# Performance work log

Hardware: AMD Instinct MI355X
Metric: run time of the kernel (lower is better)

Reference implementation:

```python
import jax, jax.numpy as jnp
import numpy as np

B, N, NODE_DIM, EDGE_DIM, HID = 32, 100, 128, 64, 128
EPS = 1e-5


def _bn(x, gamma, beta):
    # training-mode BatchNorm1d over all leading dims (biased variance)
    d = x.shape[-1]
    xf = x.reshape(-1, d)
    mean = xf.mean(axis=0)
    var = ((xf - mean) ** 2).mean(axis=0)
    return ((x - mean) * jax.lax.rsqrt(var + EPS)) * gamma + beta


def setup_inputs() -> dict:
    key = jax.random.key(0)
    ks = jax.random.split(key, 12)
    s = lambda fan_in: 1.0 / np.sqrt(fan_in)
    return {
        "h": jax.random.normal(ks[0], (B, N, NODE_DIM), jnp.float32),
        "e": jax.random.normal(ks[1], (B, N, N, EDGE_DIM), jnp.float32),
        "adj": (jax.random.uniform(ks[2], (B, N, N)) < 0.3).astype(jnp.float32),
        "WU": jax.random.uniform(ks[3], (HID, NODE_DIM), jnp.float32, -s(NODE_DIM), s(NODE_DIM)),
        "WV": jax.random.uniform(ks[4], (HID, NODE_DIM), jnp.float32, -s(NODE_DIM), s(NODE_DIM)),
        "WA": jax.random.uniform(ks[5], (HID, NODE_DIM), jnp.float32, -s(NODE_DIM), s(NODE_DIM)),
        "WB": jax.random.uniform(ks[6], (HID, NODE_DIM), jnp.float32, -s(NODE_DIM), s(NODE_DIM)),
        "WC": jax.random.uniform(ks[7], (HID, EDGE_DIM), jnp.float32, -s(EDGE_DIM), s(EDGE_DIM)),
        "bn_edge_gamma": jnp.ones((HID,), jnp.float32),
        "bn_edge_beta": jnp.zeros((HID,), jnp.float32),
        "bn_node_gamma": jnp.ones((HID,), jnp.float32),
        "bn_node_beta": jnp.zeros((HID,), jnp.float32),
    }


def reference(h, e, adj, WU, WV, WA, WB, WC,
              bn_edge_gamma, bn_edge_beta, bn_node_gamma, bn_node_beta):
    # e_new[b,m,n,d] = C(e) + A(h_m) + B(h_n)
    eh = (jnp.einsum('bmne,de->bmnd', e, WC)
          + jnp.einsum('bmc,dc->bmd', h, WA)[:, :, None, :]
          + jnp.einsum('bnc,dc->bnd', h, WB)[:, None, :, :])
    eh = jax.nn.relu(_bn(eh, bn_edge_gamma, bn_edge_beta))
    eh = eh * adj[..., None]
    e_weight = jax.nn.sigmoid(eh)
    e_norm = jax.nn.softmax(e_weight, axis=2)  # softmax over neighbor dim n
    h_in = jnp.einsum('bmc,dc->bmd', h, WU)
    h_nb = jnp.einsum('bnc,dc->bnd', h, WV)
    m = jnp.einsum('bmnd,bnd->bmd', e_norm, h_nb)
    m = _bn(m, bn_node_gamma, bn_node_beta)
    h_out = h_in + jax.nn.relu(m)
    return (h_out, e_norm)
```

## Files before the change

kernel.cpp:

```cpp
#include <hip/hip_runtime.h>
#include <math.h>

#define B_   32
#define N_   100
#define ND_  128
#define ED_  64
#define HID_ 128
#define EPS_ 1e-5f
#define NNODE (B_*N_)
#define EDGE_SAMPLES ((float)(B_*N_*N_))
#define LOG2E_ 1.4426950408889634f

#define MC_     7

#define WS_A      0
#define WS_PK     409600
#define WS_HIN    819200
#define WS_M      1638400
#define WS_STATS  2048000
#define WS_SCSH   (WS_STATS + 8192)
#define WS_NSTB   (WS_SCSH + 256)
#define ZERO_CNT  (8192 + 256 + 8192)

typedef __attribute__((ext_vector_type(8))) short bf16x8;
typedef __attribute__((ext_vector_type(4))) float f32x4;
#define MFMA16(a,b,c) __builtin_amdgcn_mfma_f32_16x16x32_bf16(a,b,c,0,0,0)

__device__ __forceinline__ unsigned short f2bf(float f) {
  unsigned int u = __float_as_uint(f);
  unsigned int r = (u + 0x7fffu + ((u >> 16) & 1u)) >> 16;
  return (unsigned short)r;
}

__global__ __launch_bounds__(256) void k1_proj(
    const float* __restrict__ h,
    const float* __restrict__ WA, const float* __restrict__ WB,
    const float* __restrict__ WU, const float* __restrict__ WV,
    float* __restrict__ ws) {
  __shared__ unsigned short h_lds[128 * 136];
  __shared__ unsigned short w_lds[128 * 136];
  const int t  = threadIdx.x;
  const int r0 = blockIdx.x * 128;
  const int y  = blockIdx.y;
  const float* W = (y == 0) ? WA : (y == 1) ? WB : (y == 2) ? WU : WV;

  {
    int gid = (y * 25 + blockIdx.x) * 256 + t;
    if (gid < ZERO_CNT) ws[WS_STATS + gid] = 0.f;
  }

  const float4* hp = (const float4*)(h + (size_t)r0 * 128);
  const float4* wp = (const float4*)W;
#pragma unroll
  for (int k = 0; k < 16; ++k) {
    int i = t + k * 256;
    int row = i >> 5, col = (i & 31) * 4;
    float4 v = hp[i];
    *(ushort4*)&h_lds[row * 136 + col] =
        make_ushort4(f2bf(v.x), f2bf(v.y), f2bf(v.z), f2bf(v.w));
    float4 u = wp[i];
    *(ushort4*)&w_lds[row * 136 + col] =
        make_ushort4(f2bf(u.x), f2bf(u.y), f2bf(u.z), f2bf(u.w));
  }
  __syncthreads();

  const int w  = t >> 6;
  const int l  = t & 63;
  const int lr = l & 15;
  const int lg = l >> 4;

  bf16x8 bfr[2][4];
#pragma unroll
  for (int nt = 0; nt < 2; ++nt) {
    int d = w * 32 + nt * 16 + lr;
#pragma unroll
    for (int kb = 0; kb < 4; ++kb)
      bfr[nt][kb] = *(const bf16x8*)&w_lds[d * 136 + kb * 32 + lg * 8];
  }

  f32x4 acc[8][2];
#pragma unroll
  for (int mt = 0; mt < 8; ++mt) { acc[mt][0] = (f32x4)0.f; acc[mt][1] = (f32x4)0.f; }

#pragma unroll
  for (int mt = 0; mt < 8; ++mt) {
    int row = mt * 16 + lr;
    bf16x8 af[4];
#pragma unroll
    for (int kb = 0; kb < 4; ++kb)
      af[kb] = *(const bf16x8*)&h_lds[row * 136 + kb * 32 + lg * 8];
#pragma unroll
    for (int nt = 0; nt < 2; ++nt)
#pragma unroll
      for (int kb = 0; kb < 4; ++kb)
        acc[mt][nt] = MFMA16(af[kb], bfr[nt][kb], acc[mt][nt]);
  }

  if (y == 0 || y == 2) {
    float* outp = ws + ((y == 0) ? WS_A : WS_HIN);
#pragma unroll
    for (int mt = 0; mt < 8; ++mt)
#pragma unroll
      for (int nt = 0; nt < 2; ++nt) {
        int dcol = w * 32 + nt * 16 + lr;
#pragma unroll
        for (int j = 0; j < 4; ++j) {
          int row = r0 + mt * 16 + lg * 4 + j;
          outp[row * 128 + dcol] = acc[mt][nt][j];
        }
      }
  } else {
    unsigned short* pks = (unsigned short*)(ws + WS_PK);
    const int half = (y == 1) ? 0 : 1;
#pragma unroll
    for (int mt = 0; mt < 8; ++mt)
#pragma unroll
      for (int nt = 0; nt < 2; ++nt) {
        int dcol = w * 32 + nt * 16 + lr;
#pragma unroll
        for (int j = 0; j < 4; ++j) {
          int row = r0 + mt * 16 + lg * 4 + j;
          pks[(row * 128 + dcol) * 2 + half] = f2bf(acc[mt][nt][j]);
        }
      }
  }
}

__global__ __launch_bounds__(256, 1) void k2_stats(
    const float* __restrict__ e, const float* __restrict__ WC,
    float* __restrict__ ws) {
  __shared__ unsigned short wc_lds[128 * 72];
  __shared__ unsigned short e_lds[2][112 * 72];
  const int t     = threadIdx.x;
  const int b     = blockIdx.x;
  const int chunk = blockIdx.y;
  const int m0    = chunk * MC_;
  const int mcnt  = min(MC_, N_ - m0);

  const float4* wcp = (const float4*)WC;
#pragma unroll
  for (int k = 0; k < 8; ++k) {
    int i = t + k * 256;
    float4 v = wcp[i];
    int row = i >> 4, col = (i & 15) * 4;
    *(ushort4*)&wc_lds[row * 72 + col] =
        make_ushort4(f2bf(v.x), f2bf(v.y), f2bf(v.z), f2bf(v.w));
  }
  for (int i = t; i < 12 * 72; i += 256) {
    e_lds[0][100 * 72 + i] = 0;
    e_lds[1][100 * 72 + i] = 0;
  }

  const int w  = t >> 6;
  const int l  = t & 63;
  const int lr = l & 15;
  const int lg = l >> 4;
  const int d0 = w * 32 + lr, d1 = d0 + 16;

  unsigned int pk0[7][4], pk1[7][4];
  const unsigned int* pkp = (const unsigned int*)(ws + WS_PK) + b * (N_ * 128);
#pragma unroll
  for (int mt = 0; mt < 7; ++mt)
#pragma unroll
    for (int j = 0; j < 4; ++j) {
      int node = mt * 16 + lg * 4 + j;
      bool ok = node < N_;
      pk0[mt][j] = ok ? pkp[node * 128 + d0] : 0u;
      pk1[mt][j] = ok ? pkp[node * 128 + d1] : 0u;
    }
  __syncthreads();

  bf16x8 bfr[2][2];
#pragma unroll
  for (int nt = 0; nt < 2; ++nt) {
    int d = w * 32 + nt * 16 + lr;
#pragma unroll
    for (int kb = 0; kb < 2; ++kb)
      bfr[nt][kb] = *(const bf16x8*)&wc_lds[d * 72 + kb * 32 + lg * 8];
  }

  float4 ld[7];
  {
    const float4* epf4 = (const float4*)(e + (size_t)(b * N_ + m0) * (N_ * ED_));
#pragma unroll
    for (int k = 0; k < 7; ++k) { int i = t + k * 256; if (i < 1600) ld[k] = epf4[i]; }
  }

  float s0 = 0.f, ss0 = 0.f, s1 = 0.f, ss1 = 0.f;
  int buf = 0;
  for (int r = 0; r < mcnt; ++r) {
#pragma unroll
    for (int k = 0; k < 7; ++k) {
      int i = t + k * 256;
      if (i < 1600) {
        float4 v = ld[k];
        int row = i >> 4, col = (i & 15) * 4;
        *(ushort4*)&e_lds[buf][row * 72 + col] =
            make_ushort4(f2bf(v.x), f2bf(v.y), f2bf(v.z), f2bf(v.w));
      }
    }
    __syncthreads();
    if (r + 1 < mcnt) {
      const float4* nxt = (const float4*)(e + (size_t)(b * N_ + m0 + r + 1) * (N_ * ED_));
#pragma unroll
      for (int k = 0; k < 7; ++k) { int i = t + k * 256; if (i < 1600) ld[k] = nxt[i]; }
    }

    const int bm = b * N_ + m0 + r;
    const float A0 = ws[WS_A + bm * 128 + d0];
    const float A1 = ws[WS_A + bm * 128 + d1];

    f32x4 acc[7][2];
#pragma unroll
    for (int mt = 0; mt < 7; ++mt) { acc[mt][0] = (f32x4)0.f; acc[mt][1] = (f32x4)0.f; }
#pragma unroll
    for (int mt = 0; mt < 7; ++mt) {
      int row = mt * 16 + lr;
      bf16x8 af0 = *(const bf16x8*)&e_lds[buf][row * 72 + lg * 8];
      bf16x8 af1 = *(const bf16x8*)&e_lds[buf][row * 72 + 32 + lg * 8];
#pragma unroll
      for (int nt = 0; nt < 2; ++nt) {
        acc[mt][nt] = MFMA16(af0, bfr[nt][0], acc[mt][nt]);
        acc[mt][nt] = MFMA16(af1, bfr[nt][1], acc[mt][nt]);
      }
    }

#pragma unroll
    for (int mt = 0; mt < 7; ++mt)
#pragma unroll
      for (int j = 0; j < 4; ++j) {
        int node = mt * 16 + lg * 4 + j;
        if (node < N_) {
          float x0 = acc[mt][0][j] + A0 + __uint_as_float(pk0[mt][j] << 16);
          float x1 = acc[mt][1][j] + A1 + __uint_as_float(pk1[mt][j] << 16);
          s0 += x0; ss0 += x0 * x0;
          s1 += x1; ss1 += x1 * x1;
        }
      }
    buf ^= 1;
  }

  s0 += __shfl_xor(s0, 16);  s0 += __shfl_xor(s0, 32);
  ss0 += __shfl_xor(ss0, 16); ss0 += __shfl_xor(ss0, 32);
  s1 += __shfl_xor(s1, 16);  s1 += __shfl_xor(s1, 32);
  ss1 += __shfl_xor(ss1, 16); ss1 += __shfl_xor(ss1, 32);
  if (l < 16) {
    atomicAdd(&ws[WS_STATS + b * 256 + d0], s0);
    atomicAdd(&ws[WS_STATS + b * 256 + 128 + d0], ss0);
    atomicAdd(&ws[WS_STATS + b * 256 + d1], s1);
    atomicAdd(&ws[WS_STATS + b * 256 + 128 + d1], ss1);
  }
}

__global__ __launch_bounds__(128) void k0_finalize(
    const float* __restrict__ gamma_e, const float* __restrict__ beta_e,
    float* __restrict__ ws) {
  const int t = threadIdx.x;
  float S = 0.f, SS = 0.f;
#pragma unroll
  for (int j = 0; j < 32; ++j) {
    S  += ws[WS_STATS + j * 256 + t];
    SS += ws[WS_STATS + j * 256 + 128 + t];
  }
  float mean = S * (1.0f / EDGE_SAMPLES);
  float var  = SS * (1.0f / EDGE_SAMPLES) - mean * mean;
  float sc   = gamma_e[t] * rsqrtf(var + EPS_);
  ws[WS_SCSH + t]       = sc;
  ws[WS_SCSH + 128 + t] = beta_e[t] - mean * sc;
}

__global__ __launch_bounds__(512) void k4_main(
    const float* __restrict__ e, const float* __restrict__ adj,
    const float* __restrict__ WC,
    float* __restrict__ ws, float* __restrict__ out_enorm) {
  __shared__ unsigned short e_lds[112 * 72];
  __shared__ float adj_lds[112];
  const int t  = threadIdx.x;
  const int bm = blockIdx.x;
  const int b  = bm / N_;
  const int w  = t >> 6;
  const int l  = t & 63;
  const int lr = l & 15;
  const int lg = l >> 4;
  const int d0 = w * 16 + lr;

  float4 ld[4];
  const float4* ef4 = (const float4*)(e + (size_t)bm * (N_ * ED_));
#pragma unroll
  for (int k = 0; k < 4; ++k) { int i = t + k * 512; if (i < 1600) ld[k] = ef4[i]; }

  unsigned int pk[7][4];
  const unsigned int* pkp = (const unsigned int*)(ws + WS_PK) + b * (N_ * 128);
#pragma unroll
  for (int mt = 0; mt < 7; ++mt)
#pragma unroll
    for (int j = 0; j < 4; ++j) {
      int node = mt * 16 + lg * 4 + j;
      pk[mt][j] = (node < N_) ? pkp[node * 128 + d0] : 0u;
    }
  const float A0  = ws[WS_A + bm * 128 + d0];
  const float sc0 = ws[WS_SCSH + d0];
  const float sh0 = ws[WS_SCSH + 128 + d0];

  bf16x8 bfr[2];
#pragma unroll
  for (int kb = 0; kb < 2; ++kb) {
    const float* wrow = WC + d0 * 64 + kb * 32 + lg * 8;
    float4 u0 = *(const float4*)wrow;
    float4 u1 = *(const float4*)(wrow + 4);
    bf16x8 f;
    f[0] = (short)f2bf(u0.x); f[1] = (short)f2bf(u0.y);
    f[2] = (short)f2bf(u0.z); f[3] = (short)f2bf(u0.w);
    f[4] = (short)f2bf(u1.x); f[5] = (short)f2bf(u1.y);
    f[6] = (short)f2bf(u1.z); f[7] = (short)f2bf(u1.w);
    bfr[kb] = f;
  }

  if (t < 112) adj_lds[t] = (t < N_) ? adj[bm * N_ + t] : 0.f;

#pragma unroll
  for (int k = 0; k < 4; ++k) {
    int i = t + k * 512;
    if (i < 1600) {
      float4 v = ld[k];
      int row = i >> 4, col = (i & 15) * 4;
      *(ushort4*)&e_lds[row * 72 + col] =
          make_ushort4(f2bf(v.x), f2bf(v.y), f2bf(v.z), f2bf(v.w));
    }
  }
  for (int i = t; i < 12 * 72; i += 512) e_lds[100 * 72 + i] = 0;
  __syncthreads();

  f32x4 acc[7];
#pragma unroll
  for (int mt = 0; mt < 7; ++mt) acc[mt] = (f32x4)0.f;
#pragma unroll
  for (int mt = 0; mt < 7; ++mt) {
    int row = mt * 16 + lr;
    bf16x8 af0 = *(const bf16x8*)&e_lds[row * 72 + lg * 8];
    bf16x8 af1 = *(const bf16x8*)&e_lds[row * 72 + 32 + lg * 8];
    acc[mt] = MFMA16(af0, bfr[0], acc[mt]);
    acc[mt] = MFMA16(af1, bfr[1], acc[mt]);
  }

  float den = 0.f;
#pragma unroll
  for (int mt = 0; mt < 7; ++mt)
#pragma unroll
    for (int j = 0; j < 4; ++j) {
      int node = mt * 16 + lg * 4 + j;
      float bv = __uint_as_float(pk[mt][j] << 16);
      float x  = (acc[mt][j] + A0 + bv) * sc0 + sh0;
      float r  = fmaxf(x, 0.f) * adj_lds[node];
      float en = __builtin_amdgcn_exp2f(r * -LOG2E_);
      float sg = __builtin_amdgcn_rcpf(1.f + en);
      float p  = __builtin_amdgcn_exp2f(sg * LOG2E_);
      acc[mt][j] = p; den += p;
    }
  den += __shfl_xor(den, 16); den += __shfl_xor(den, 32);
  den -= 12.f * __builtin_amdgcn_exp2f(0.5f * LOG2E_);
  const float rc = __builtin_amdgcn_rcpf(den);

  float msg = 0.f;
  float* outp = out_enorm + (size_t)bm * (N_ * 128);
#pragma unroll
  for (int mt = 0; mt < 7; ++mt)
#pragma unroll
    for (int j = 0; j < 4; ++j) {
      int node = mt * 16 + lg * 4 + j;
      if (node < N_) {
        float v = acc[mt][j] * rc;
        outp[node * 128 + d0] = v;
        float hn = __uint_as_float(pk[mt][j] & 0xffff0000u);
        msg += v * hn;
      }
    }
  msg += __shfl_xor(msg, 16); msg += __shfl_xor(msg, 32);
  if (l < 16) {
    ws[WS_M + bm * 128 + d0] = msg;
    atomicAdd(&ws[WS_NSTB + b * 256 + d0],       msg);
    atomicAdd(&ws[WS_NSTB + b * 256 + 128 + d0], msg * msg);
  }
}

__global__ __launch_bounds__(256) void k5b_hout(
    const float* __restrict__ gamma_n, const float* __restrict__ beta_n,
    const float* __restrict__ ws, float* __restrict__ hout) {
  __shared__ float sc_l[128], sh_l[128];
  const int t = threadIdx.x;
  if (t < 128) {
    float S = 0.f, SS = 0.f;
#pragma unroll
    for (int j = 0; j < 32; ++j) {
      S  += ws[WS_NSTB + j * 256 + t];
      SS += ws[WS_NSTB + j * 256 + 128 + t];
    }
    float mean = S * (1.0f / (float)NNODE);
    float var  = SS * (1.0f / (float)NNODE) - mean * mean;
    float sc   = gamma_n[t] * rsqrtf(var + EPS_);
    sc_l[t] = sc;
    sh_l[t] = beta_n[t] - mean * sc;
  }
  __syncthreads();
  const int idx = blockIdx.x * 256 + t;
  const int d = t & 127;
  float mv = ws[WS_M + idx];
  hout[idx] = ws[WS_HIN + idx] + fmaxf(mv * sc_l[d] + sh_l[d], 0.f);
}

extern "C" void kernel_launch(void* const* d_in, const int* in_sizes, int n_in,
                              void* d_out, int out_size, void* d_ws, size_t ws_size,
                              hipStream_t stream) {
  (void)in_sizes; (void)n_in; (void)out_size; (void)ws_size;
  const float* h   = (const float*)d_in[0];
  const float* e   = (const float*)d_in[1];
  const float* adj = (const float*)d_in[2];
  const float* WU  = (const float*)d_in[3];
  const float* WV  = (const float*)d_in[4];
  const float* WA  = (const float*)d_in[5];
  const float* WB  = (const float*)d_in[6];
  const float* WC  = (const float*)d_in[7];
  const float* geg = (const float*)d_in[8];
  const float* geb = (const float*)d_in[9];
  const float* gng = (const float*)d_in[10];
  const float* gnb = (const float*)d_in[11];

  float* out = (float*)d_out;
  float* ws  = (float*)d_ws;

  k1_proj    <<<dim3(25, 4),  256, 0, stream>>>(h, WA, WB, WU, WV, ws);
  k2_stats   <<<dim3(32, 15), 256, 0, stream>>>(e, WC, ws);
  k0_finalize<<<1,            128, 0, stream>>>(geg, geb, ws);
  k4_main    <<<3200,         512, 0, stream>>>(e, adj, WC, ws, out + 409600);
  k5b_hout   <<<1600,         256, 0, stream>>>(gng, gnb, ws, out);
}
```

Measured before the change: 89.09 us.

## Regrid stats and projection kernels for more parallelism and swizzle main block order

The stats kernel changes from 480 blocks of 256 threads, each looping over 7 rows with both 32-wide halves of the hidden dimension per wave, to 1600 blocks of 512 threads that each handle two rows with 16 hidden columns per wave. WC is loaded straight from global memory rather than staged through LDS. The projection kernel halves its row tile to 64 so it launches twice as many blocks. The main kernel remaps block indices in a strided swizzle across batches, meant to spread work across XCDs and caches. The aim is better occupancy and latency hiding on the bandwidth-bound pass over e, at the cost of more blocks, more redundant loads of pk, A and WC, and more atomics.

```diff
diff --git a/kernel.cpp b/kernel.cpp
--- a/kernel.cpp
+++ b/kernel.cpp
@@ -11,8 +11,6 @@
 #define EDGE_SAMPLES ((float)(B_*N_*N_))
 #define LOG2E_ 1.4426950408889634f
 
-#define MC_     7
-
 #define WS_A      0
 #define WS_PK     409600
 #define WS_HIN    819200
@@ -32,277 +30,8 @@
   return (unsigned short)r;
 }
 
-__global__ __launch_bounds__(256) void k1_proj(
-    const float* __restrict__ h,
-    const float* __restrict__ WA, const float* __restrict__ WB,
-    const float* __restrict__ WU, const float* __restrict__ WV,
-    float* __restrict__ ws) {
-  __shared__ unsigned short h_lds[128 * 136];
-  __shared__ unsigned short w_lds[128 * 136];
-  const int t  = threadIdx.x;
-  const int r0 = blockIdx.x * 128;
-  const int y  = blockIdx.y;
-  const float* W = (y == 0) ? WA : (y == 1) ? WB : (y == 2) ? WU : WV;
-
-  {
-    int gid = (y * 25 + blockIdx.x) * 256 + t;
-    if (gid < ZERO_CNT) ws[WS_STATS + gid] = 0.f;
-  }
-
-  const float4* hp = (const float4*)(h + (size_t)r0 * 128);
-  const float4* wp = (const float4*)W;
-#pragma unroll
-  for (int k = 0; k < 16; ++k) {
-    int i = t + k * 256;
-    int row = i >> 5, col = (i & 31) * 4;
-    float4 v = hp[i];
-    *(ushort4*)&h_lds[row * 136 + col] =
-        make_ushort4(f2bf(v.x), f2bf(v.y), f2bf(v.z), f2bf(v.w));
-    float4 u = wp[i];
-    *(ushort4*)&w_lds[row * 136 + col] =
-        make_ushort4(f2bf(u.x), f2bf(u.y), f2bf(u.z), f2bf(u.w));
-  }
-  __syncthreads();
-
-  const int w  = t >> 6;
-  const int l  = t & 63;
-  const int lr = l & 15;
-  const int lg = l >> 4;
-
-  bf16x8 bfr[2][4];
-#pragma unroll
-  for (int nt = 0; nt < 2; ++nt) {
-    int d = w * 32 + nt * 16 + lr;
-#pragma unroll
-    for (int kb = 0; kb < 4; ++kb)
-      bfr[nt][kb] = *(const bf16x8*)&w_lds[d * 136 + kb * 32 + lg * 8];
-  }
-
-  f32x4 acc[8][2];
-#pragma unroll
-  for (int mt = 0; mt < 8; ++mt) { acc[mt][0] = (f32x4)0.f; acc[mt][1] = (f32x4)0.f; }
-
-#pragma unroll
-  for (int mt = 0; mt < 8; ++mt) {
-    int row = mt * 16 + lr;
-    bf16x8 af[4];
-#pragma unroll
-    for (int kb = 0; kb < 4; ++kb)
-      af[kb] = *(const bf16x8*)&h_lds[row * 136 + kb * 32 + lg * 8];
-#pragma unroll
-    for (int nt = 0; nt < 2; ++nt)
-#pragma unroll
-      for (int kb = 0; kb < 4; ++kb)
-        acc[mt][nt] = MFMA16(af[kb], bfr[nt][kb], acc[mt][nt]);
-  }
-
-  if (y == 0 || y == 2) {
-    float* outp = ws + ((y == 0) ? WS_A : WS_HIN);
-#pragma unroll
-    for (int mt = 0; mt < 8; ++mt)
-#pragma unroll
-      for (int nt = 0; nt < 2; ++nt) {
-        int dcol = w * 32 + nt * 16 + lr;
-#pragma unroll
-        for (int j = 0; j < 4; ++j) {
-          int row = r0 + mt * 16 + lg * 4 + j;
-          outp[row * 128 + dcol] = acc[mt][nt][j];
-        }
-      }
-  } else {
-    unsigned short* pks = (unsigned short*)(ws + WS_PK);
-    const int half = (y == 1) ? 0 : 1;
-#pragma unroll
-    for (int mt = 0; mt < 8; ++mt)
-#pragma unroll
-      for (int nt = 0; nt < 2; ++nt) {
-        int dcol = w * 32 + nt * 16 + lr;
-#pragma unroll
-        for (int j = 0; j < 4; ++j) {
-          int row = r0 + mt * 16 + lg * 4 + j;
-          pks[(row * 128 + dcol) * 2 + half] = f2bf(acc[mt][nt][j]);
-        }
-      }
-  }
-}
-
-__global__ __launch_bounds__(256, 1) void k2_stats(
-    const float* __restrict__ e, const float* __restrict__ WC,
-    float* __restrict__ ws) {
-  __shared__ unsigned short wc_lds[128 * 72];
-  __shared__ unsigned short e_lds[2][112 * 72];
-  const int t     = threadIdx.x;
-  const int b     = blockIdx.x;
-  const int chunk = blockIdx.y;
-  const int m0    = chunk * MC_;
-  const int mcnt  = min(MC_, N_ - m0);
-
-  const float4* wcp = (const float4*)WC;
-#pragma unroll
-  for (int k = 0; k < 8; ++k) {
-    int i = t + k * 256;
-    float4 v = wcp[i];
-    int row = i >> 4, col = (i & 15) * 4;
-    *(ushort4*)&wc_lds[row * 72 + col] =
-        make_ushort4(f2bf(v.x), f2bf(v.y), f2bf(v.z), f2bf(v.w));
-  }
-  for (int i = t; i < 12 * 72; i += 256) {
-    e_lds[0][100 * 72 + i] = 0;
-    e_lds[1][100 * 72 + i] = 0;
-  }
-
-  const int w  = t >> 6;
-  const int l  = t & 63;
-  const int lr = l & 15;
-  const int lg = l >> 4;
-  const int d0 = w * 32 + lr, d1 = d0 + 16;
-
-  unsigned int pk0[7][4], pk1[7][4];
-  const unsigned int* pkp = (const unsigned int*)(ws + WS_PK) + b * (N_ * 128);
-#pragma unroll
-  for (int mt = 0; mt < 7; ++mt)
-#pragma unroll
-    for (int j = 0; j < 4; ++j) {
-      int node = mt * 16 + lg * 4 + j;
-      bool ok = node < N_;
-      pk0[mt][j] = ok ? pkp[node * 128 + d0] : 0u;
-      pk1[mt][j] = ok ? pkp[node * 128 + d1] : 0u;
-    }
-  __syncthreads();
-
-  bf16x8 bfr[2][2];
-#pragma unroll
-  for (int nt = 0; nt < 2; ++nt) {
-    int d = w * 32 + nt * 16 + lr;
-#pragma unroll
-    for (int kb = 0; kb < 2; ++kb)
-      bfr[nt][kb] = *(const bf16x8*)&wc_lds[d * 72 + kb * 32 + lg * 8];
-  }
-
-  float4 ld[7];
-  {
-    const float4* epf4 = (const float4*)(e + (size_t)(b * N_ + m0) * (N_ * ED_));
-#pragma unroll
-    for (int k = 0; k < 7; ++k) { int i = t + k * 256; if (i < 1600) ld[k] = epf4[i]; }
-  }
-
-  float s0 = 0.f, ss0 = 0.f, s1 = 0.f, ss1 = 0.f;
-  int buf = 0;
-  for (int r = 0; r < mcnt; ++r) {
-#pragma unroll
-    for (int k = 0; k < 7; ++k) {
-      int i = t + k * 256;
-      if (i < 1600) {
-        float4 v = ld[k];
-        int row = i >> 4, col = (i & 15) * 4;
-        *(ushort4*)&e_lds[buf][row * 72 + col] =
-            make_ushort4(f2bf(v.x), f2bf(v.y), f2bf(v.z), f2bf(v.w));
-      }
-    }
-    __syncthreads();
-    if (r + 1 < mcnt) {
-      const float4* nxt = (const float4*)(e + (size_t)(b * N_ + m0 + r + 1) * (N_ * ED_));
-#pragma unroll
-      for (int k = 0; k < 7; ++k) { int i = t + k * 256; if (i < 1600) ld[k] = nxt[i]; }
-    }
-
-    const int bm = b * N_ + m0 + r;
-    const float A0 = ws[WS_A + bm * 128 + d0];
-    const float A1 = ws[WS_A + bm * 128 + d1];
-
-    f32x4 acc[7][2];
-#pragma unroll
-    for (int mt = 0; mt < 7; ++mt) { acc[mt][0] = (f32x4)0.f; acc[mt][1] = (f32x4)0.f; }
-#pragma unroll
-    for (int mt = 0; mt < 7; ++mt) {
-      int row = mt * 16 + lr;
-      bf16x8 af0 = *(const bf16x8*)&e_lds[buf][row * 72 + lg * 8];
-      bf16x8 af1 = *(const bf16x8*)&e_lds[buf][row * 72 + 32 + lg * 8];
-#pragma unroll
-      for (int nt = 0; nt < 2; ++nt) {
-        acc[mt][nt] = MFMA16(af0, bfr[nt][0], acc[mt][nt]);
-        acc[mt][nt] = MFMA16(af1, bfr[nt][1], acc[mt][nt]);
-      }
-    }
-
-#pragma unroll
-    for (int mt = 0; mt < 7; ++mt)
-#pragma unroll
-      for (int j = 0; j < 4; ++j) {
-        int node = mt * 16 + lg * 4 + j;
-        if (node < N_) {
-          float x0 = acc[mt][0][j] + A0 + __uint_as_float(pk0[mt][j] << 16);
-          float x1 = acc[mt][1][j] + A1 + __uint_as_float(pk1[mt][j] << 16);
-          s0 += x0; ss0 += x0 * x0;
-          s1 += x1; ss1 += x1 * x1;
-        }
-      }
-    buf ^= 1;
-  }
-
-  s0 += __shfl_xor(s0, 16);  s0 += __shfl_xor(s0, 32);
-  ss0 += __shfl_xor(ss0, 16); ss0 += __shfl_xor(ss0, 32);
-  s1 += __shfl_xor(s1, 16);  s1 += __shfl_xor(s1, 32);
-  ss1 += __shfl_xor(ss1, 16); ss1 += __shfl_xor(ss1, 32);
-  if (l < 16) {
-    atomicAdd(&ws[WS_STATS + b * 256 + d0], s0);
-    atomicAdd(&ws[WS_STATS + b * 256 + 128 + d0], ss0);
-    atomicAdd(&ws[WS_STATS + b * 256 + d1], s1);
-    atomicAdd(&ws[WS_STATS + b * 256 + 128 + d1], ss1);
-  }
-}
-
-__global__ __launch_bounds__(128) void k0_finalize(
-    const float* __restrict__ gamma_e, const float* __restrict__ beta_e,
-    float* __restrict__ ws) {
-  const int t = threadIdx.x;
-  float S = 0.f, SS = 0.f;
-#pragma unroll
-  for (int j = 0; j < 32; ++j) {
-    S  += ws[WS_STATS + j * 256 + t];
-    SS += ws[WS_STATS + j * 256 + 128 + t];
-  }
-  float mean = S * (1.0f / EDGE_SAMPLES);
-  float var  = SS * (1.0f / EDGE_SAMPLES) - mean * mean;
-  float sc   = gamma_e[t] * rsqrtf(var + EPS_);
-  ws[WS_SCSH + t]       = sc;
-  ws[WS_SCSH + 128 + t] = beta_e[t] - mean * sc;
-}
-
-__global__ __launch_bounds__(512) void k4_main(
-    const float* __restrict__ e, const float* __restrict__ adj,
-    const float* __restrict__ WC,
-    float* __restrict__ ws, float* __restrict__ out_enorm) {
-  __shared__ unsigned short e_lds[112 * 72];
-  __shared__ float adj_lds[112];
-  const int t  = threadIdx.x;
-  const int bm = blockIdx.x;
-  const int b  = bm / N_;
-  const int w  = t >> 6;
-  const int l  = t & 63;
-  const int lr = l & 15;
-  const int lg = l >> 4;
-  const int d0 = w * 16 + lr;
-
-  float4 ld[4];
-  const float4* ef4 = (const float4*)(e + (size_t)bm * (N_ * ED_));
-#pragma unroll
-  for (int k = 0; k < 4; ++k) { int i = t + k * 512; if (i < 1600) ld[k] = ef4[i]; }
-
-  unsigned int pk[7][4];
-  const unsigned int* pkp = (const unsigned int*)(ws + WS_PK) + b * (N_ * 128);
-#pragma unroll
-  for (int mt = 0; mt < 7; ++mt)
-#pragma unroll
-    for (int j = 0; j < 4; ++j) {
-      int node = mt * 16 + lg * 4 + j;
-      pk[mt][j] = (node < N_) ? pkp[node * 128 + d0] : 0u;
-    }
-  const float A0  = ws[WS_A + bm * 128 + d0];
-  const float sc0 = ws[WS_SCSH + d0];
-  const float sh0 = ws[WS_SCSH + 128 + d0];
-
-  bf16x8 bfr[2];
+__device__ __forceinline__ void load_wc_frags(const float* __restrict__ WC,
+                                              int d0, int lg, bf16x8 bfr[2]) {
 #pragma unroll
   for (int kb = 0; kb < 2; ++kb) {
     const float* wrow = WC + d0 * 64 + kb * 32 + lg * 8;
@@ -315,33 +44,278 @@
     f[6] = (short)f2bf(u1.z); f[7] = (short)f2bf(u1.w);
     bfr[kb] = f;
   }
-
-  if (t < 112) adj_lds[t] = (t < N_) ? adj[bm * N_ + t] : 0.f;
-
+}
+
+__device__ __forceinline__ void stage_row512(const float4 ld[4],
+                                             unsigned short* dst, int t) {
 #pragma unroll
   for (int k = 0; k < 4; ++k) {
     int i = t + k * 512;
     if (i < 1600) {
       float4 v = ld[k];
       int row = i >> 4, col = (i & 15) * 4;
-      *(ushort4*)&e_lds[row * 72 + col] =
+      *(ushort4*)&dst[row * 72 + col] =
           make_ushort4(f2bf(v.x), f2bf(v.y), f2bf(v.z), f2bf(v.w));
     }
   }
+}
+
+__device__ __forceinline__ void mfma_row(const unsigned short* src,
+                                         const bf16x8 bfr[2], f32x4 acc[7],
+                                         int lr, int lg) {
+#pragma unroll
+  for (int mt = 0; mt < 7; ++mt) {
+    int row = mt * 16 + lr;
+    bf16x8 af0 = *(const bf16x8*)&src[row * 72 + lg * 8];
+    bf16x8 af1 = *(const bf16x8*)&src[row * 72 + 32 + lg * 8];
+    f32x4 a = (f32x4)0.f;
+    a = MFMA16(af0, bfr[0], a);
+    a = MFMA16(af1, bfr[1], a);
+    acc[mt] = a;
+  }
+}
+
+__global__ __launch_bounds__(256) void k1_proj(
+    const float* __restrict__ h,
+    const float* __restrict__ WA, const float* __restrict__ WB,
+    const float* __restrict__ WU, const float* __restrict__ WV,
+    float* __restrict__ ws) {
+  __shared__ unsigned short h_lds[64 * 136];
+  __shared__ unsigned short w_lds[128 * 136];
+  const int t  = threadIdx.x;
+  const int r0 = blockIdx.x * 64;
+  const int y  = blockIdx.y;
+  const float* W = (y == 0) ? WA : (y == 1) ? WB : (y == 2) ? WU : WV;
+
+  {
+    int gid = (y * 50 + blockIdx.x) * 256 + t;
+    if (gid < ZERO_CNT) ws[WS_STATS + gid] = 0.f;
+  }
+
+  const float4* hp = (const float4*)(h + (size_t)r0 * 128);
+  const float4* wp = (const float4*)W;
+#pragma unroll
+  for (int k = 0; k < 8; ++k) {
+    int i = t + k * 256;
+    int row = i >> 5, col = (i & 31) * 4;
+    float4 v = hp[i];
+    *(ushort4*)&h_lds[row * 136 + col] =
+        make_ushort4(f2bf(v.x), f2bf(v.y), f2bf(v.z), f2bf(v.w));
+  }
+#pragma unroll
+  for (int k = 0; k < 16; ++k) {
+    int i = t + k * 256;
+    int row = i >> 5, col = (i & 31) * 4;
+    float4 u = wp[i];
+    *(ushort4*)&w_lds[row * 136 + col] =
+        make_ushort4(f2bf(u.x), f2bf(u.y), f2bf(u.z), f2bf(u.w));
+  }
+  __syncthreads();
+
+  const int w  = t >> 6;
+  const int l  = t & 63;
+  const int lr = l & 15;
+  const int lg = l >> 4;
+
+  bf16x8 bfr[2][4];
+#pragma unroll
+  for (int nt = 0; nt < 2; ++nt) {
+    int d = w * 32 + nt * 16 + lr;
+#pragma unroll
+    for (int kb = 0; kb < 4; ++kb)
+      bfr[nt][kb] = *(const bf16x8*)&w_lds[d * 136 + kb * 32 + lg * 8];
+  }
+
+  f32x4 acc[4][2];
+#pragma unroll
+  for (int mt = 0; mt < 4; ++mt) { acc[mt][0] = (f32x4)0.f; acc[mt][1] = (f32x4)0.f; }
+
+#pragma unroll
+  for (int mt = 0; mt < 4; ++mt) {
+    int row = mt * 16 + lr;
+    bf16x8 af[4];
+#pragma unroll
+    for (int kb = 0; kb < 4; ++kb)
+      af[kb] = *(const bf16x8*)&h_lds[row * 136 + kb * 32 + lg * 8];
+#pragma unroll
+    for (int nt = 0; nt < 2; ++nt)
+#pragma unroll
+      for (int kb = 0; kb < 4; ++kb)
+        acc[mt][nt] = MFMA16(af[kb], bfr[nt][kb], acc[mt][nt]);
+  }
+
+  if (y == 0 || y == 2) {
+    float* outp = ws + ((y == 0) ? WS_A : WS_HIN);
+#pragma unroll
+    for (int mt = 0; mt < 4; ++mt)
+#pragma unroll
+      for (int nt = 0; nt < 2; ++nt) {
+        int dcol = w * 32 + nt * 16 + lr;
+#pragma unroll
+        for (int j = 0; j < 4; ++j) {
+          int row = r0 + mt * 16 + lg * 4 + j;
+          outp[row * 128 + dcol] = acc[mt][nt][j];
+        }
+      }
+  } else {
+    unsigned short* pks = (unsigned short*)(ws + WS_PK);
+    const int half = (y == 1) ? 0 : 1;
+#pragma unroll
+    for (int mt = 0; mt < 4; ++mt)
+#pragma unroll
+      for (int nt = 0; nt < 2; ++nt) {
+        int dcol = w * 32 + nt * 16 + lr;
+#pragma unroll
+        for (int j = 0; j < 4; ++j) {
+          int row = r0 + mt * 16 + lg * 4 + j;
+          pks[(row * 128 + dcol) * 2 + half] = f2bf(acc[mt][nt][j]);
+        }
+      }
+  }
+}
+
+__global__ __launch_bounds__(512) void k2_stats(
+    const float* __restrict__ e, const float* __restrict__ WC,
+    float* __restrict__ ws) {
+  __shared__ unsigned short e_lds[2][112 * 72];
+  const int t   = threadIdx.x;
+  const int b   = blockIdx.x;
+  const int bm0 = b * N_ + blockIdx.y * 2;
+  const int w   = t >> 6;
+  const int l   = t & 63;
+  const int lr  = l & 15;
+  const int lg  = l >> 4;
+  const int d0  = w * 16 + lr;
+
+  float4 ld[4];
+  const float4* e0 = (const float4*)(e + (size_t)bm0 * (N_ * ED_));
+#pragma unroll
+  for (int k = 0; k < 4; ++k) { int i = t + k * 512; if (i < 1600) ld[k] = e0[i]; }
+
+  unsigned int pk[7][4];
+  const unsigned int* pkp = (const unsigned int*)(ws + WS_PK) + b * (N_ * 128);
+#pragma unroll
+  for (int mt = 0; mt < 7; ++mt)
+#pragma unroll
+    for (int j = 0; j < 4; ++j) {
+      int node = mt * 16 + lg * 4 + j;
+      pk[mt][j] = (node < N_) ? pkp[node * 128 + d0] : 0u;
+    }
+  const float Aa = ws[WS_A + bm0 * 128 + d0];
+  const float Ab = ws[WS_A + (bm0 + 1) * 128 + d0];
+
+  bf16x8 bfr[2];
+  load_wc_frags(WC, d0, lg, bfr);
+
+  for (int i = t; i < 12 * 72; i += 512) {
+    e_lds[0][100 * 72 + i] = 0;
+    e_lds[1][100 * 72 + i] = 0;
+  }
+
+  stage_row512(ld, e_lds[0], t);
+  const float4* e1 = (const float4*)(e + (size_t)(bm0 + 1) * (N_ * ED_));
+#pragma unroll
+  for (int k = 0; k < 4; ++k) { int i = t + k * 512; if (i < 1600) ld[k] = e1[i]; }
+  __syncthreads();
+
+  f32x4 acc[7];
+  float s = 0.f, ssq = 0.f;
+
+  mfma_row(e_lds[0], bfr, acc, lr, lg);
+  stage_row512(ld, e_lds[1], t);
+#pragma unroll
+  for (int mt = 0; mt < 7; ++mt)
+#pragma unroll
+    for (int j = 0; j < 4; ++j) {
+      int node = mt * 16 + lg * 4 + j;
+      if (node < N_) {
+        float x = acc[mt][j] + Aa + __uint_as_float(pk[mt][j] << 16);
+        s += x; ssq += x * x;
+      }
+    }
+  __syncthreads();
+
+  mfma_row(e_lds[1], bfr, acc, lr, lg);
+#pragma unroll
+  for (int mt = 0; mt < 7; ++mt)
+#pragma unroll
+    for (int j = 0; j < 4; ++j) {
+      int node = mt * 16 + lg * 4 + j;
+      if (node < N_) {
+        float x = acc[mt][j] + Ab + __uint_as_float(pk[mt][j] << 16);
+        s += x; ssq += x * x;
+      }
+    }
+
+  s   += __shfl_xor(s, 16);   s   += __shfl_xor(s, 32);
+  ssq += __shfl_xor(ssq, 16); ssq += __shfl_xor(ssq, 32);
+  if (l < 16) {
+    atomicAdd(&ws[WS_STATS + b * 256 + d0], s);
+    atomicAdd(&ws[WS_STATS + b * 256 + 128 + d0], ssq);
+  }
+}
+
+__global__ __launch_bounds__(128) void k0_finalize(
+    const float* __restrict__ gamma_e, const float* __restrict__ beta_e,
+    float* __restrict__ ws) {
+  const int t = threadIdx.x;
+  float S = 0.f, SS = 0.f;
+#pragma unroll
+  for (int j = 0; j < 32; ++j) {
+    S  += ws[WS_STATS + j * 256 + t];
+    SS += ws[WS_STATS + j * 256 + 128 + t];
+  }
+  float mean = S * (1.0f / EDGE_SAMPLES);
+  float var  = SS * (1.0f / EDGE_SAMPLES) - mean * mean;
+  float sc   = gamma_e[t] * rsqrtf(var + EPS_);
+  ws[WS_SCSH + t]       = sc;
+  ws[WS_SCSH + 128 + t] = beta_e[t] - mean * sc;
+}
+
+__global__ __launch_bounds__(512) void k4_main(
+    const float* __restrict__ e, const float* __restrict__ adj,
+    const float* __restrict__ WC,
+    float* __restrict__ ws, float* __restrict__ out_enorm) {
+  __shared__ unsigned short e_lds[112 * 72];
+  __shared__ float adj_lds[112];
+  const int t  = threadIdx.x;
+  const int bm = (blockIdx.x & 7) * 400 + (blockIdx.x >> 3);
+  const int b  = bm / N_;
+  const int w  = t >> 6;
+  const int l  = t & 63;
+  const int lr = l & 15;
+  const int lg = l >> 4;
+  const int d0 = w * 16 + lr;
+
+  float4 ld[4];
+  const float4* ef4 = (const float4*)(e + (size_t)bm * (N_ * ED_));
+#pragma unroll
+  for (int k = 0; k < 4; ++k) { int i = t + k * 512; if (i < 1600) ld[k] = ef4[i]; }
+
+  unsigned int pk[7][4];
+  const unsigned int* pkp = (const unsigned int*)(ws + WS_PK) + b * (N_ * 128);
+#pragma unroll
+  for (int mt = 0; mt < 7; ++mt)
+#pragma unroll
+    for (int j = 0; j < 4; ++j) {
+      int node = mt * 16 + lg * 4 + j;
+      pk[mt][j] = (node < N_) ? pkp[node * 128 + d0] : 0u;
+    }
+  const float A0  = ws[WS_A + bm * 128 + d0];
+  const float sc0 = ws[WS_SCSH + d0];
+  const float sh0 = ws[WS_SCSH + 128 + d0];
+
+  bf16x8 bfr[2];
+  load_wc_frags(WC, d0, lg, bfr);
+
+  if (t < 112) adj_lds[t] = (t < N_) ? adj[bm * N_ + t] : 0.f;
+
+  stage_row512(ld, e_lds, t);
   for (int i = t; i < 12 * 72; i += 512) e_lds[100 * 72 + i] = 0;
   __syncthreads();
 
   f32x4 acc[7];
-#pragma unroll
-  for (int mt = 0; mt < 7; ++mt) acc[mt] = (f32x4)0.f;
-#pragma unroll
-  for (int mt = 0; mt < 7; ++mt) {
-    int row = mt * 16 + lr;
-    bf16x8 af0 = *(const bf16x8*)&e_lds[row * 72 + lg * 8];
-    bf16x8 af1 = *(const bf16x8*)&e_lds[row * 72 + 32 + lg * 8];
-    acc[mt] = MFMA16(af0, bfr[0], acc[mt]);
-    acc[mt] = MFMA16(af1, bfr[1], acc[mt]);
-  }
+  mfma_row(e_lds, bfr, acc, lr, lg);
 
   float den = 0.f;
 #pragma unroll
@@ -428,8 +402,8 @@
   float* out = (float*)d_out;
   float* ws  = (float*)d_ws;
 
-  k1_proj    <<<dim3(25, 4),  256, 0, stream>>>(h, WA, WB, WU, WV, ws);
-  k2_stats   <<<dim3(32, 15), 256, 0, stream>>>(e, WC, ws);
+  k1_proj    <<<dim3(50, 4),  256, 0, stream>>>(h, WA, WB, WU, WV, ws);
+  k2_stats   <<<dim3(32, 50), 512, 0, stream>>>(e, WC, ws);
   k0_finalize<<<1,            128, 0, stream>>>(geg, geb, ws);
   k4_main    <<<3200,         512, 0, stream>>>(e, adj, WC, ws, out + 409600);
   k5b_hout   <<<1600,         256, 0, stream>>>(gng, gnb, ws, out);
```

Result: slower. 97.21 us (+9.1%).

## Cache bf16-converted edge tensor in workspace for reuse by main kernel

Applied to the files above, without the earlier changes.

The stats kernel now writes its bf16-converted copy of e into a workspace buffer. The main kernel reads this half-size copy instead of re-reading fp32 e and converting it again. This halves the second pass's read traffic on the large edge tensor, at the cost of an extra bf16 write pass in the stats kernel. The WC fragment load moves into a helper and the MFMA accumulator init is restructured, both cosmetic.

```diff
diff --git a/kernel.cpp b/kernel.cpp
--- a/kernel.cpp
+++ b/kernel.cpp
@@ -11,7 +11,7 @@
 #define EDGE_SAMPLES ((float)(B_*N_*N_))
 #define LOG2E_ 1.4426950408889634f
 
-#define MC_     7
+#define MC_   7
 
 #define WS_A      0
 #define WS_PK     409600
@@ -20,6 +20,7 @@
 #define WS_STATS  2048000
 #define WS_SCSH   (WS_STATS + 8192)
 #define WS_NSTB   (WS_SCSH + 256)
+#define WS_EC     2064640
 #define ZERO_CNT  (8192 + 256 + 8192)
 
 typedef __attribute__((ext_vector_type(8))) short bf16x8;
@@ -30,6 +31,22 @@
   unsigned int u = __float_as_uint(f);
   unsigned int r = (u + 0x7fffu + ((u >> 16) & 1u)) >> 16;
   return (unsigned short)r;
+}
+
+__device__ __forceinline__ void load_wc_frags(const float* __restrict__ WC,
+                                              int d0, int lg, bf16x8 bfr[2]) {
+#pragma unroll
+  for (int kb = 0; kb < 2; ++kb) {
+    const float* wrow = WC + d0 * 64 + kb * 32 + lg * 8;
+    float4 u0 = *(const float4*)wrow;
+    float4 u1 = *(const float4*)(wrow + 4);
+    bf16x8 f;
+    f[0] = (short)f2bf(u0.x); f[1] = (short)f2bf(u0.y);
+    f[2] = (short)f2bf(u0.z); f[3] = (short)f2bf(u0.w);
+    f[4] = (short)f2bf(u1.x); f[5] = (short)f2bf(u1.y);
+    f[6] = (short)f2bf(u1.z); f[7] = (short)f2bf(u1.w);
+    bfr[kb] = f;
+  }
 }
 
 __global__ __launch_bounds__(256) void k1_proj(
@@ -186,17 +203,21 @@
     for (int k = 0; k < 7; ++k) { int i = t + k * 256; if (i < 1600) ld[k] = epf4[i]; }
   }
 
+  unsigned short* ec = (unsigned short*)(ws + WS_EC);
+
   float s0 = 0.f, ss0 = 0.f, s1 = 0.f, ss1 = 0.f;
   int buf = 0;
   for (int r = 0; r < mcnt; ++r) {
+    unsigned short* ecp = ec + (size_t)(b * N_ + m0 + r) * 6400;
 #pragma unroll
     for (int k = 0; k < 7; ++k) {
       int i = t + k * 256;
       if (i < 1600) {
         float4 v = ld[k];
+        ushort4 p4 = make_ushort4(f2bf(v.x), f2bf(v.y), f2bf(v.z), f2bf(v.w));
         int row = i >> 4, col = (i & 15) * 4;
-        *(ushort4*)&e_lds[buf][row * 72 + col] =
-            make_ushort4(f2bf(v.x), f2bf(v.y), f2bf(v.z), f2bf(v.w));
+        *(ushort4*)&e_lds[buf][row * 72 + col] = p4;
+        *(ushort4*)&ecp[i * 4] = p4;
       }
     }
     __syncthreads();
@@ -270,8 +291,7 @@
 }
 
 __global__ __launch_bounds__(512) void k4_main(
-    const float* __restrict__ e, const float* __restrict__ adj,
-    const float* __restrict__ WC,
+    const float* __restrict__ adj, const float* __restrict__ WC,
     float* __restrict__ ws, float* __restrict__ out_enorm) {
   __shared__ unsigned short e_lds[112 * 72];
   __shared__ float adj_lds[112];
@@ -284,10 +304,11 @@
   const int lg = l >> 4;
   const int d0 = w * 16 + lr;
 
-  float4 ld[4];
-  const float4* ef4 = (const float4*)(e + (size_t)bm * (N_ * ED_));
-#pragma unroll
-  for (int k = 0; k < 4; ++k) { int i = t + k * 512; if (i < 1600) ld[k] = ef4[i]; }
+  ushort4 ld[4];
+  const ushort4* ef = (const ushort4*)((const unsigned short*)(ws + WS_EC)
+                                       + (size_t)bm * 6400);
+#pragma unroll
+  for (int k = 0; k < 4; ++k) { int i = t + k * 512; if (i < 1600) ld[k] = ef[i]; }
 
   unsigned int pk[7][4];
   const unsigned int* pkp = (const unsigned int*)(ws + WS_PK) + b * (N_ * 128);
@@ -303,18 +324,7 @@
   const float sh0 = ws[WS_SCSH + 128 + d0];
 
   bf16x8 bfr[2];
-#pragma unroll
-  for (int kb = 0; kb < 2; ++kb) {
-    const float* wrow = WC + d0 * 64 + kb * 32 + lg * 8;
-    float4 u0 = *(const float4*)wrow;
-    float4 u1 = *(const float4*)(wrow + 4);
-    bf16x8 f;
-    f[0] = (short)f2bf(u0.x); f[1] = (short)f2bf(u0.y);
-    f[2] = (short)f2bf(u0.z); f[3] = (short)f2bf(u0.w);
-    f[4] = (short)f2bf(u1.x); f[5] = (short)f2bf(u1.y);
-    f[6] = (short)f2bf(u1.z); f[7] = (short)f2bf(u1.w);
-    bfr[kb] = f;
-  }
+  load_wc_frags(WC, d0, lg, bfr);
 
   if (t < 112) adj_lds[t] = (t < N_) ? adj[bm * N_ + t] : 0.f;
 
@@ -322,25 +332,23 @@
   for (int k = 0; k < 4; ++k) {
     int i = t + k * 512;
     if (i < 1600) {
-      float4 v = ld[k];
       int row = i >> 4, col = (i & 15) * 4;
-      *(ushort4*)&e_lds[row * 72 + col] =
-          make_ushort4(f2bf(v.x), f2bf(v.y), f2bf(v.z), f2bf(v.w));
+      *(ushort4*)&e_lds[row * 72 + col] = ld[k];
     }
   }
   for (int i = t; i < 12 * 72; i += 512) e_lds[100 * 72 + i] = 0;
   __syncthreads();
 
   f32x4 acc[7];
-#pragma unroll
-  for (int mt = 0; mt < 7; ++mt) acc[mt] = (f32x4)0.f;
 #pragma unroll
   for (int mt = 0; mt < 7; ++mt) {
     int row = mt * 16 + lr;
     bf16x8 af0 = *(const bf16x8*)&e_lds[row * 72 + lg * 8];
     bf16x8 af1 = *(const bf16x8*)&e_lds[row * 72 + 32 + lg * 8];
-    acc[mt] = MFMA16(af0, bfr[0], acc[mt]);
-    acc[mt] = MFMA16(af1, bfr[1], acc[mt]);
+    f32x4 a = (f32x4)0.f;
+    a = MFMA16(af0, bfr[0], a);
+    a = MFMA16(af1, bfr[1], a);
+    acc[mt] = a;
   }
 
   float den = 0.f;
@@ -431,6 +439,6 @@
   k1_proj    <<<dim3(25, 4),  256, 0, stream>>>(h, WA, WB, WU, WV, ws);
   k2_stats   <<<dim3(32, 15), 256, 0, stream>>>(e, WC, ws);
   k0_finalize<<<1,            128, 0, stream>>>(geg, geb, ws);
-  k4_main    <<<3200,         512, 0, stream>>>(e, adj, WC, ws, out + 409600);
+  k4_main    <<<3200,         512, 0, stream>>>(adj, WC, ws, out + 409600);
   k5b_hout   <<<1600,         256, 0, stream>>>(gng, gnb, ws, out);
 }
```

New measurement: 101.1 us. 13.5% more time.
